# Performance work log

Measured on AMD Instinct MI355X. Metric: run time of the kernel, lower is better.

The kernel has to match this reference:

```python
import jax, jax.numpy as jnp
import numpy as np

B, T, D, H, C = 64, 256, 512, 1024, 1000

def setup_inputs() -> dict:
    key = jax.random.key(0)
    ks = jax.random.split(key, 6)
    s = 1.0 / np.sqrt(H)  # torch nn.RNN init scale
    return {
        "x": jax.random.normal(ks[0], (B, T, D), dtype=jnp.float32),
        "w_ih0": jax.random.normal(ks[1], (H, D), dtype=jnp.float32) * s,
        "w_hh0": jax.random.normal(ks[2], (H, H), dtype=jnp.float32) * s,
        "w_ih1": jax.random.normal(ks[3], (H, H), dtype=jnp.float32) * s,
        "w_hh1": jax.random.normal(ks[4], (H, H), dtype=jnp.float32) * s,
        "w_fc": jax.random.normal(ks[5], (C, H), dtype=jnp.float32) * s,
    }

def _rnn_layer(inp, w_ih, w_hh):
    # inp: [B, T, Din]; ReLU RNN, no bias (matches nn.RNN(nonlinearity='relu', bias=False))
    xs = jnp.einsum('btd,hd->tbh', inp, w_ih)  # precompute input projections for all steps
    h0 = jnp.zeros((inp.shape[0], w_hh.shape[0]), dtype=inp.dtype)
    def step(h, x_t):
        h = jax.nn.relu(x_t + h @ w_hh.T)
        return h, h
    _, ys = jax.lax.scan(step, h0, xs)  # ys: [T, B, H]
    return jnp.swapaxes(ys, 0, 1)  # [B, T, H]

def reference(x, w_ih0, w_hh0, w_ih1, w_hh1, w_fc):
    h1 = _rnn_layer(x, w_ih0, w_hh0)
    h2 = _rnn_layer(h1, w_ih1, w_hh1)
    # fc on last timestep, no bias
    return h2[:, -1, :] @ w_fc.T  # [B, C]
```

## Files before the change

kernel.cpp:

```cpp
#include <hip/hip_runtime.h>

#define T_STEPS 256
#define BATCH   64
#define HID     1024
#define DIN     512
#define NCLS    1000
#define NBLK    128
#define HSZ     (BATCH * HID)

typedef __attribute__((ext_vector_type(8))) short  short8;
typedef __attribute__((ext_vector_type(4))) float  f32x4;
typedef unsigned long long u64;

__device__ __forceinline__ unsigned short rne_bf16(float f) {
    unsigned int u = __builtin_bit_cast(unsigned int, f);
    u += 0x7FFFu + ((u >> 16) & 1u);
    return (unsigned short)(u >> 16);
}
__device__ __forceinline__ float bf16_to_f(unsigned short h) {
    unsigned int u = ((unsigned int)h) << 16;
    return __builtin_bit_cast(float, u);
}

#define MFMA(a, b, c) __builtin_amdgcn_mfma_f32_16x16x32_bf16((a), (b), (c), 0, 0, 0)

__device__ __forceinline__ short8 ld_st8(const unsigned short* p) {
    u64 a = __hip_atomic_load((const u64*)p,       __ATOMIC_RELAXED, __HIP_MEMORY_SCOPE_AGENT);
    u64 b = __hip_atomic_load((const u64*)(p + 4), __ATOMIC_RELAXED, __HIP_MEMORY_SCOPE_AGENT);
    union { u64 q[2]; short8 v; } u;
    u.q[0] = a; u.q[1] = b;
    return u.v;
}
__device__ __forceinline__ void st_u32(unsigned short* p, unsigned int v) {
    __hip_atomic_store((unsigned int*)p, v, __ATOMIC_RELAXED, __HIP_MEMORY_SCOPE_AGENT);
}

__device__ __forceinline__ void grid_bar(int* cnt, int bid, int tid, int p) {
    __syncthreads();
    if (tid == 0) {
        __hip_atomic_fetch_add(&cnt[((bid >> 1) & 7) * 32], 1,
                               __ATOMIC_RELAXED, __HIP_MEMORY_SCOPE_AGENT);
        const int target = 64 * (p + 1);
        for (long it = 0; it < 50000000L; ++it) {
            int s = 0;
#pragma unroll
            for (int i = 0; i < 8; ++i)
                s += __hip_atomic_load(&cnt[i * 32], __ATOMIC_RELAXED,
                                       __HIP_MEMORY_SCOPE_AGENT);
            if (s >= target) break;
        }
        asm volatile("" ::: "memory");
    }
    __syncthreads();
}

__device__ __forceinline__ void reduce_store(const float* red, int tid,
                                             int mbase, int nbase,
                                             unsigned short* ohi, unsigned short* olo,
                                             float* of, const float* xp) {
    const int m = tid >> 4;
    const int n = (tid * 2) & 31;
    float s0, s1;
    if (xp) {
        float2 xi = *(const float2*)(xp + (size_t)(mbase + m) * HID + nbase + n);
        s0 = xi.x; s1 = xi.y;
    } else { s0 = 0.f; s1 = 0.f; }
#pragma unroll
    for (int ww = 0; ww < 8; ++ww) {
        const float* rp = red + ww * 1088 + m * 34 + n;
        s0 += rp[0];
        s1 += rp[1];
    }
    const float v0 = fmaxf(s0, 0.f), v1 = fmaxf(s1, 0.f);
    const unsigned short h0 = rne_bf16(v0), h1 = rne_bf16(v1);
    const unsigned int hp = (unsigned int)h0 | ((unsigned int)h1 << 16);
    const unsigned int lp = (unsigned int)rne_bf16(v0 - bf16_to_f(h0)) |
                            ((unsigned int)rne_bf16(v1 - bf16_to_f(h1)) << 16);
    const size_t o = (size_t)(mbase + m) * HID + nbase + n;
    st_u32(ohi + o, hp);
    st_u32(olo + o, lp);
    if (of) { float2 f2; f2.x = v0; f2.y = v1; *(float2*)(of + o) = f2; }
}

__global__ __launch_bounds__(512, 2)
void rnn_mfma(const float* __restrict__ xproj,
              const unsigned short* __restrict__ whh0h, const unsigned short* __restrict__ whh0l,
              const unsigned short* __restrict__ wih1h, const unsigned short* __restrict__ wih1l,
              const unsigned short* __restrict__ whh1h, const unsigned short* __restrict__ whh1l,
              unsigned short* h1hi, unsigned short* h1lo,
              unsigned short* h2hi, unsigned short* h2lo,
              float* h2f, int* bar) {
    __shared__ float red[8 * 1088];

    const int bid   = blockIdx.x;
    const int z     = bid >> 6;
    const int r     = bid & 63;
    const int nbase = (r >> 1) * 32;
    const int mbase = (r & 1) * 32;
    const int tid   = threadIdx.x;
    const int w     = tid >> 6;
    const int lane  = tid & 63;
    const int l15   = lane & 15;
    const int kq    = (lane >> 4) * 8;

    int* cnt = bar + (bid & 1) * 256;

    if (z == 0) {
        short8 WH[2][4], WL[2][4];
        const int kb = w * 128;
#pragma unroll
        for (int c = 0; c < 4; ++c)
#pragma unroll
            for (int nt = 0; nt < 2; ++nt) {
                const size_t o = (size_t)(nbase + nt * 16 + l15) * HID + kb + c * 32 + kq;
                WH[nt][c] = *(const short8*)(whh0h + o);
                WL[nt][c] = *(const short8*)(whh0l + o);
            }
        for (int p = 0; p <= T_STEPS; ++p) {
            if (p < T_STEPS) {
                f32x4 acc[2][2] = {};
                const unsigned short* hch = h1hi + (size_t)(p & 1) * HSZ;
                const unsigned short* hcl = h1lo + (size_t)(p & 1) * HSZ;
#pragma unroll
                for (int c = 0; c < 4; ++c) {
                    short8 ah[2], al[2];
#pragma unroll
                    for (int mt = 0; mt < 2; ++mt) {
                        const size_t o = (size_t)(mbase + mt * 16 + l15) * HID + kb + c * 32 + kq;
                        ah[mt] = ld_st8(hch + o);
                        al[mt] = ld_st8(hcl + o);
                    }
#pragma unroll
                    for (int mt = 0; mt < 2; ++mt)
#pragma unroll
                        for (int nt = 0; nt < 2; ++nt) {
                            acc[mt][nt] = MFMA(ah[mt], WH[nt][c], acc[mt][nt]);
                            acc[mt][nt] = MFMA(al[mt], WH[nt][c], acc[mt][nt]);
                            acc[mt][nt] = MFMA(ah[mt], WL[nt][c], acc[mt][nt]);
                        }
                }
#pragma unroll
                for (int mt = 0; mt < 2; ++mt)
#pragma unroll
                    for (int nt = 0; nt < 2; ++nt)
#pragma unroll
                        for (int i = 0; i < 4; ++i)
                            red[w * 1088 + (mt * 16 + (lane >> 4) * 4 + i) * 34 +
                                nt * 16 + l15] = acc[mt][nt][i];
                __syncthreads();
                const size_t ob = (size_t)((p + 1) & 1) * HSZ;
                reduce_store(red, tid, mbase, nbase, h1hi + ob, h1lo + ob, nullptr,
                             xproj + (size_t)p * BATCH * HID);
            }
            grid_bar(cnt, bid, tid, p);
        }
    } else {
        short8 WH[2][8], WL[2][8];
        const unsigned short* ph = (w < 4) ? wih1h : whh1h;
        const unsigned short* pl = (w < 4) ? wih1l : whh1l;
        const int kb = (w & 3) * 256;
#pragma unroll
        for (int c = 0; c < 8; ++c)
#pragma unroll
            for (int nt = 0; nt < 2; ++nt) {
                const size_t o = (size_t)(nbase + nt * 16 + l15) * HID + kb + c * 32 + kq;
                WH[nt][c] = *(const short8*)(ph + o);
                WL[nt][c] = *(const short8*)(pl + o);
            }
        for (int p = 0; p <= T_STEPS; ++p) {
            if (p >= 1) {
                f32x4 acc[2][2] = {};
                const unsigned short* ash = (w < 4) ? h1hi + (size_t)(p & 1) * HSZ
                                                    : h2hi + (size_t)((p - 1) & 1) * HSZ;
                const unsigned short* asl = (w < 4) ? h1lo + (size_t)(p & 1) * HSZ
                                                    : h2lo + (size_t)((p - 1) & 1) * HSZ;
#pragma unroll
                for (int c = 0; c < 8; ++c) {
                    short8 ah[2], al[2];
#pragma unroll
                    for (int mt = 0; mt < 2; ++mt) {
                        const size_t o = (size_t)(mbase + mt * 16 + l15) * HID + kb + c * 32 + kq;
                        ah[mt] = ld_st8(ash + o);
                        al[mt] = ld_st8(asl + o);
                    }
#pragma unroll
                    for (int mt = 0; mt < 2; ++mt)
#pragma unroll
                        for (int nt = 0; nt < 2; ++nt) {
                            acc[mt][nt] = MFMA(ah[mt], WH[nt][c], acc[mt][nt]);
                            acc[mt][nt] = MFMA(al[mt], WH[nt][c], acc[mt][nt]);
                            acc[mt][nt] = MFMA(ah[mt], WL[nt][c], acc[mt][nt]);
                        }
                }
#pragma unroll
                for (int mt = 0; mt < 2; ++mt)
#pragma unroll
                    for (int nt = 0; nt < 2; ++nt)
#pragma unroll
                        for (int i = 0; i < 4; ++i)
                            red[w * 1088 + (mt * 16 + (lane >> 4) * 4 + i) * 34 +
                                nt * 16 + l15] = acc[mt][nt][i];
                __syncthreads();
                const size_t ob = (size_t)(p & 1) * HSZ;
                reduce_store(red, tid, mbase, nbase, h2hi + ob, h2lo + ob,
                             (p == T_STEPS) ? h2f : nullptr, nullptr);
            }
            grid_bar(cnt, bid, tid, p);
        }
    }
}

__global__ __launch_bounds__(512)
void xproj_gemm(const float* __restrict__ x,
                const unsigned short* __restrict__ wh,
                const unsigned short* __restrict__ wl,
                float* __restrict__ xproj) {
    const int t    = blockIdx.x;
    const int nq   = blockIdx.y;
    const int w    = threadIdx.x >> 6;
    const int lane = threadIdx.x & 63;
    const int l15  = lane & 15;
    const int kq   = (lane >> 4) * 8;
    const int n0   = nq * 256 + w * 32;

    f32x4 acc[4][2] = {};
    for (int c = 0; c < 16; ++c) {
        const int k = c * 32 + kq;
        short8 wfh[2], wfl[2];
#pragma unroll
        for (int nt = 0; nt < 2; ++nt) {
            const size_t o = (size_t)(n0 + nt * 16 + l15) * DIN + k;
            wfh[nt] = *(const short8*)(wh + o);
            wfl[nt] = *(const short8*)(wl + o);
        }
#pragma unroll
        for (int mt = 0; mt < 4; ++mt) {
            const float* xr = x + ((size_t)(mt * 16 + l15) * T_STEPS + t) * DIN + k;
            float4 a0 = *(const float4*)xr;
            float4 a1 = *(const float4*)(xr + 4);
            float f[8] = {a0.x, a0.y, a0.z, a0.w, a1.x, a1.y, a1.z, a1.w};
            short8 ah, al;
#pragma unroll
            for (int i = 0; i < 8; ++i) {
                unsigned short h = rne_bf16(f[i]);
                ah[i] = (short)h;
                al[i] = (short)rne_bf16(f[i] - bf16_to_f(h));
            }
#pragma unroll
            for (int nt = 0; nt < 2; ++nt) {
                acc[mt][nt] = MFMA(ah, wfh[nt], acc[mt][nt]);
                acc[mt][nt] = MFMA(al, wfh[nt], acc[mt][nt]);
                acc[mt][nt] = MFMA(ah, wfl[nt], acc[mt][nt]);
            }
        }
    }
    float* op = xproj + (size_t)t * BATCH * HID;
#pragma unroll
    for (int mt = 0; mt < 4; ++mt)
#pragma unroll
        for (int nt = 0; nt < 2; ++nt)
#pragma unroll
            for (int i = 0; i < 4; ++i) {
                const int m = mt * 16 + (lane >> 4) * 4 + i;
                const int n = n0 + nt * 16 + l15;
                op[(size_t)m * HID + n] = acc[mt][nt][i];
            }
}

__global__ void split_w(const float* __restrict__ src,
                        unsigned short* __restrict__ hi,
                        unsigned short* __restrict__ lo, int n) {
    int i = blockIdx.x * 256 + threadIdx.x;
    if (i < n) {
        float v = src[i];
        unsigned short h = rne_bf16(v);
        hi[i] = h;
        lo[i] = rne_bf16(v - bf16_to_f(h));
    }
}

__global__ void zero_kernel(int* __restrict__ p, int n) {
    int i = blockIdx.x * 256 + threadIdx.x;
    if (i < n) p[i] = 0;
}

__global__ void fc_kernel(const float* __restrict__ h2,
                          const float* __restrict__ w_fc,
                          float* __restrict__ out) {
    __shared__ float hs[HID];
    const int b = blockIdx.x;
    for (int i = threadIdx.x; i < HID; i += 256) hs[i] = h2[(size_t)b * HID + i];
    __syncthreads();
    const int c = blockIdx.y * 256 + threadIdx.x;
    if (c < NCLS) {
        const float* w = w_fc + (size_t)c * HID;
        float s = 0.f;
        for (int k = 0; k < HID; k += 4) {
            float4 wv = *(const float4*)(w + k);
            s += wv.x * hs[k] + wv.y * hs[k + 1] + wv.z * hs[k + 2] + wv.w * hs[k + 3];
        }
        out[(size_t)b * NCLS + c] = s;
    }
}

extern "C" void kernel_launch(void* const* d_in, const int* in_sizes, int n_in,
                              void* d_out, int out_size, void* d_ws, size_t ws_size,
                              hipStream_t stream) {
    const float* x     = (const float*)d_in[0];
    const float* w_ih0 = (const float*)d_in[1];
    const float* w_hh0 = (const float*)d_in[2];
    const float* w_ih1 = (const float*)d_in[3];
    const float* w_hh1 = (const float*)d_in[4];
    const float* w_fc  = (const float*)d_in[5];
    float* out = (float*)d_out;

    char* ws = (char*)d_ws;
    size_t off = 0;
    auto alloc = [&](size_t bytes) { char* p = ws + off; off += bytes; return p; };
    float*          xproj = (float*)alloc((size_t)T_STEPS * BATCH * HID * 4);
    unsigned short* wih0h = (unsigned short*)alloc((size_t)DIN * HID * 2);
    unsigned short* wih0l = (unsigned short*)alloc((size_t)DIN * HID * 2);
    unsigned short* whh0h = (unsigned short*)alloc((size_t)HID * HID * 2);
    unsigned short* whh0l = (unsigned short*)alloc((size_t)HID * HID * 2);
    unsigned short* wih1h = (unsigned short*)alloc((size_t)HID * HID * 2);
    unsigned short* wih1l = (unsigned short*)alloc((size_t)HID * HID * 2);
    unsigned short* whh1h = (unsigned short*)alloc((size_t)HID * HID * 2);
    unsigned short* whh1l = (unsigned short*)alloc((size_t)HID * HID * 2);
    unsigned short* h1hi  = (unsigned short*)alloc(2 * HSZ * 2);
    unsigned short* h1lo  = (unsigned short*)alloc(2 * HSZ * 2);
    unsigned short* h2hi  = (unsigned short*)alloc(2 * HSZ * 2);
    unsigned short* h2lo  = (unsigned short*)alloc(2 * HSZ * 2);
    float*          h2f   = (float*)alloc(HSZ * 4);
    int*            bar   = (int*)alloc(4096);

    split_w<<<(DIN * HID + 255) / 256, 256, 0, stream>>>(w_ih0, wih0h, wih0l, DIN * HID);
    split_w<<<(HID * HID + 255) / 256, 256, 0, stream>>>(w_hh0, whh0h, whh0l, HID * HID);
    split_w<<<(HID * HID + 255) / 256, 256, 0, stream>>>(w_ih1, wih1h, wih1l, HID * HID);
    split_w<<<(HID * HID + 255) / 256, 256, 0, stream>>>(w_hh1, whh1h, whh1l, HID * HID);

    xproj_gemm<<<dim3(T_STEPS, 4), 512, 0, stream>>>(x, wih0h, wih0l, xproj);

    const int nzero = (4 * (2 * HSZ * 2) + HSZ * 4 + 4096) / 4;
    zero_kernel<<<(nzero + 255) / 256, 256, 0, stream>>>((int*)h1hi, nzero);

    rnn_mfma<<<NBLK, 512, 0, stream>>>(xproj,
                                       whh0h, whh0l,
                                       wih1h, wih1l, whh1h, whh1l,
                                       h1hi, h1lo, h2hi, h2lo, h2f, bar);

    fc_kernel<<<dim3(64, 4), 256, 0, stream>>>(h2f, w_fc, out);
}
```

Baseline: 4.445 ms.

## Replace global grid barrier with per-batch-chunk dataflow counters in persistent RNN

Replaces the per-step global grid barrier with per-chunk arrival counters, splitting the batch into four chunks of 16 rows. Each block now waits only on the counters for the chunk it is about to compute, so layers and blocks can run ahead in a wavefront. Tiles shrink from 32x32 to 16 columns by 16 rows per chunk, and spin-waits use s_sleep. This trades more synchronisation events, smaller MFMA tiles and repeated activation reloads for less barrier stall and more overlap between layers.

After: 8.339 ms. 87.6% more time.

```diff
diff --git a/kernel.cpp b/kernel.cpp
--- a/kernel.cpp
+++ b/kernel.cpp
@@ -6,6 +6,7 @@
 #define DIN     512
 #define NCLS    1000
 #define NBLK    128
+#define NCH     4
 #define HSZ     (BATCH * HID)
 
 typedef __attribute__((ext_vector_type(8))) short  short8;
@@ -35,51 +36,22 @@
     __hip_atomic_store((unsigned int*)p, v, __ATOMIC_RELAXED, __HIP_MEMORY_SCOPE_AGENT);
 }
 
-__device__ __forceinline__ void grid_bar(int* cnt, int bid, int tid, int p) {
-    __syncthreads();
-    if (tid == 0) {
-        __hip_atomic_fetch_add(&cnt[((bid >> 1) & 7) * 32], 1,
-                               __ATOMIC_RELAXED, __HIP_MEMORY_SCOPE_AGENT);
-        const int target = 64 * (p + 1);
-        for (long it = 0; it < 50000000L; ++it) {
-            int s = 0;
-#pragma unroll
-            for (int i = 0; i < 8; ++i)
-                s += __hip_atomic_load(&cnt[i * 32], __ATOMIC_RELAXED,
-                                       __HIP_MEMORY_SCOPE_AGENT);
-            if (s >= target) break;
-        }
-        asm volatile("" ::: "memory");
-    }
-    __syncthreads();
-}
-
-__device__ __forceinline__ void reduce_store(const float* red, int tid,
-                                             int mbase, int nbase,
-                                             unsigned short* ohi, unsigned short* olo,
-                                             float* of, const float* xp) {
-    const int m = tid >> 4;
-    const int n = (tid * 2) & 31;
-    float s0, s1;
-    if (xp) {
-        float2 xi = *(const float2*)(xp + (size_t)(mbase + m) * HID + nbase + n);
-        s0 = xi.x; s1 = xi.y;
-    } else { s0 = 0.f; s1 = 0.f; }
-#pragma unroll
-    for (int ww = 0; ww < 8; ++ww) {
-        const float* rp = red + ww * 1088 + m * 34 + n;
-        s0 += rp[0];
-        s1 += rp[1];
-    }
-    const float v0 = fmaxf(s0, 0.f), v1 = fmaxf(s1, 0.f);
-    const unsigned short h0 = rne_bf16(v0), h1 = rne_bf16(v1);
-    const unsigned int hp = (unsigned int)h0 | ((unsigned int)h1 << 16);
-    const unsigned int lp = (unsigned int)rne_bf16(v0 - bf16_to_f(h0)) |
-                            ((unsigned int)rne_bf16(v1 - bf16_to_f(h1)) << 16);
-    const size_t o = (size_t)(mbase + m) * HID + nbase + n;
-    st_u32(ohi + o, hp);
-    st_u32(olo + o, lp);
-    if (of) { float2 f2; f2.x = v0; f2.y = v1; *(float2*)(of + o) = f2; }
+__device__ __forceinline__ void wait_ge(const int* a, const int* b, int tgt) {
+    for (long it = 0; it < 100000000L; ++it) {
+        int s1 = 0, s2 = 0;
+#pragma unroll
+        for (int i = 0; i < 4; ++i) {
+            s1 += __hip_atomic_load(a + i * 16, __ATOMIC_RELAXED, __HIP_MEMORY_SCOPE_AGENT);
+            s2 += __hip_atomic_load(b + i * 16, __ATOMIC_RELAXED, __HIP_MEMORY_SCOPE_AGENT);
+        }
+        if (s1 >= tgt && s2 >= tgt) break;
+        __builtin_amdgcn_s_sleep(2);
+    }
+    asm volatile("" ::: "memory");
+}
+__device__ __forceinline__ void arrive(int* cb, int bid) {
+    __hip_atomic_fetch_add(cb + (bid & 3) * 16, 1,
+                           __ATOMIC_RELAXED, __HIP_MEMORY_SCOPE_AGENT);
 }
 
 __global__ __launch_bounds__(512, 2)
@@ -90,122 +62,147 @@
               unsigned short* h1hi, unsigned short* h1lo,
               unsigned short* h2hi, unsigned short* h2lo,
               float* h2f, int* bar) {
-    __shared__ float red[8 * 1088];
-
-    const int bid   = blockIdx.x;
-    const int z     = bid >> 6;
-    const int r     = bid & 63;
-    const int nbase = (r >> 1) * 32;
-    const int mbase = (r & 1) * 32;
-    const int tid   = threadIdx.x;
-    const int w     = tid >> 6;
-    const int lane  = tid & 63;
-    const int l15   = lane & 15;
-    const int kq    = (lane >> 4) * 8;
-
-    int* cnt = bar + (bid & 1) * 256;
-
-    if (z == 0) {
-        short8 WH[2][4], WL[2][4];
+    __shared__ float red[8][16][18];
+
+    const int bid  = blockIdx.x;
+    const int tid  = threadIdx.x;
+    const int w    = tid >> 6;
+    const int lane = tid & 63;
+    const int l15  = lane & 15;
+    const int kq   = (lane >> 4) * 8;
+    const int rm   = tid >> 3;
+    const int rn   = (tid & 7) * 2;
+
+    int* C1[NCH];
+    int* C2[NCH];
+#pragma unroll
+    for (int ch = 0; ch < NCH; ++ch) {
+        C1[ch] = bar + ch * 64;
+        C2[ch] = bar + (NCH + ch) * 64;
+    }
+
+    if (bid < 64) {
+        const int nb = bid * 16;
         const int kb = w * 128;
-#pragma unroll
-        for (int c = 0; c < 4; ++c)
-#pragma unroll
-            for (int nt = 0; nt < 2; ++nt) {
-                const size_t o = (size_t)(nbase + nt * 16 + l15) * HID + kb + c * 32 + kq;
-                WH[nt][c] = *(const short8*)(whh0h + o);
-                WL[nt][c] = *(const short8*)(whh0l + o);
-            }
-        for (int p = 0; p <= T_STEPS; ++p) {
-            if (p < T_STEPS) {
-                f32x4 acc[2][2] = {};
-                const unsigned short* hch = h1hi + (size_t)(p & 1) * HSZ;
-                const unsigned short* hcl = h1lo + (size_t)(p & 1) * HSZ;
-#pragma unroll
-                for (int c = 0; c < 4; ++c) {
-                    short8 ah[2], al[2];
-#pragma unroll
-                    for (int mt = 0; mt < 2; ++mt) {
-                        const size_t o = (size_t)(mbase + mt * 16 + l15) * HID + kb + c * 32 + kq;
-                        ah[mt] = ld_st8(hch + o);
-                        al[mt] = ld_st8(hcl + o);
+        short8 WH[4], WL[4];
+#pragma unroll
+        for (int ci = 0; ci < 4; ++ci) {
+            const size_t o = (size_t)(nb + l15) * HID + kb + ci * 32 + kq;
+            WH[ci] = *(const short8*)(whh0h + o);
+            WL[ci] = *(const short8*)(whh0l + o);
+        }
+        for (int p = 0; p < T_STEPS; ++p) {
+            const unsigned short* hch = h1hi + (size_t)(p & 1) * HSZ;
+            const unsigned short* hcl = h1lo + (size_t)(p & 1) * HSZ;
+            unsigned short* ohi = h1hi + (size_t)((p + 1) & 1) * HSZ;
+            unsigned short* olo = h1lo + (size_t)((p + 1) & 1) * HSZ;
+            const float* xp = xproj + (size_t)p * BATCH * HID;
+            for (int ch = 0; ch < NCH; ++ch) {
+                if (p > 0) {
+                    if (tid == 0) wait_ge(C1[ch], C2[ch], 64 * p);
+                    __syncthreads();
+                }
+                float2 xi = make_float2(0.f, 0.f);
+                if (tid < 128)
+                    xi = *(const float2*)(xp + (size_t)(ch * 16 + rm) * HID + nb + rn);
+                f32x4 acc = {};
+#pragma unroll
+                for (int ci = 0; ci < 4; ++ci) {
+                    const size_t o = (size_t)(ch * 16 + l15) * HID + kb + ci * 32 + kq;
+                    short8 ah = ld_st8(hch + o);
+                    short8 al = ld_st8(hcl + o);
+                    acc = MFMA(ah, WH[ci], acc);
+                    acc = MFMA(al, WH[ci], acc);
+                    acc = MFMA(ah, WL[ci], acc);
+                }
+#pragma unroll
+                for (int i = 0; i < 4; ++i)
+                    red[w][(lane >> 4) * 4 + i][l15] = acc[i];
+                __syncthreads();
+                if (tid < 128) {
+                    float s0 = xi.x, s1 = xi.y;
+#pragma unroll
+                    for (int ww = 0; ww < 8; ++ww) {
+                        s0 += red[ww][rm][rn];
+                        s1 += red[ww][rm][rn + 1];
                     }
-#pragma unroll
-                    for (int mt = 0; mt < 2; ++mt)
-#pragma unroll
-                        for (int nt = 0; nt < 2; ++nt) {
-                            acc[mt][nt] = MFMA(ah[mt], WH[nt][c], acc[mt][nt]);
-                            acc[mt][nt] = MFMA(al[mt], WH[nt][c], acc[mt][nt]);
-                            acc[mt][nt] = MFMA(ah[mt], WL[nt][c], acc[mt][nt]);
-                        }
-                }
-#pragma unroll
-                for (int mt = 0; mt < 2; ++mt)
-#pragma unroll
-                    for (int nt = 0; nt < 2; ++nt)
-#pragma unroll
-                        for (int i = 0; i < 4; ++i)
-                            red[w * 1088 + (mt * 16 + (lane >> 4) * 4 + i) * 34 +
-                                nt * 16 + l15] = acc[mt][nt][i];
-                __syncthreads();
-                const size_t ob = (size_t)((p + 1) & 1) * HSZ;
-                reduce_store(red, tid, mbase, nbase, h1hi + ob, h1lo + ob, nullptr,
-                             xproj + (size_t)p * BATCH * HID);
-            }
-            grid_bar(cnt, bid, tid, p);
+                    const float v0 = fmaxf(s0, 0.f), v1 = fmaxf(s1, 0.f);
+                    const unsigned short h0 = rne_bf16(v0), h1 = rne_bf16(v1);
+                    const unsigned int hp = (unsigned int)h0 | ((unsigned int)h1 << 16);
+                    const unsigned int lp = (unsigned int)rne_bf16(v0 - bf16_to_f(h0)) |
+                                            ((unsigned int)rne_bf16(v1 - bf16_to_f(h1)) << 16);
+                    const size_t o = (size_t)(ch * 16 + rm) * HID + nb + rn;
+                    st_u32(ohi + o, hp);
+                    st_u32(olo + o, lp);
+                }
+                __syncthreads();
+                if (tid == 0) arrive(C1[ch], bid);
+            }
         }
     } else {
-        short8 WH[2][8], WL[2][8];
+        const int nb = (bid - 64) * 16;
         const unsigned short* ph = (w < 4) ? wih1h : whh1h;
         const unsigned short* pl = (w < 4) ? wih1l : whh1l;
         const int kb = (w & 3) * 256;
-#pragma unroll
-        for (int c = 0; c < 8; ++c)
-#pragma unroll
-            for (int nt = 0; nt < 2; ++nt) {
-                const size_t o = (size_t)(nbase + nt * 16 + l15) * HID + kb + c * 32 + kq;
-                WH[nt][c] = *(const short8*)(ph + o);
-                WL[nt][c] = *(const short8*)(pl + o);
-            }
-        for (int p = 0; p <= T_STEPS; ++p) {
-            if (p >= 1) {
-                f32x4 acc[2][2] = {};
-                const unsigned short* ash = (w < 4) ? h1hi + (size_t)(p & 1) * HSZ
-                                                    : h2hi + (size_t)((p - 1) & 1) * HSZ;
-                const unsigned short* asl = (w < 4) ? h1lo + (size_t)(p & 1) * HSZ
-                                                    : h2lo + (size_t)((p - 1) & 1) * HSZ;
-#pragma unroll
-                for (int c = 0; c < 8; ++c) {
-                    short8 ah[2], al[2];
-#pragma unroll
-                    for (int mt = 0; mt < 2; ++mt) {
-                        const size_t o = (size_t)(mbase + mt * 16 + l15) * HID + kb + c * 32 + kq;
-                        ah[mt] = ld_st8(ash + o);
-                        al[mt] = ld_st8(asl + o);
+        short8 WH[8], WL[8];
+#pragma unroll
+        for (int ci = 0; ci < 8; ++ci) {
+            const size_t o = (size_t)(nb + l15) * HID + kb + ci * 32 + kq;
+            WH[ci] = *(const short8*)(ph + o);
+            WL[ci] = *(const short8*)(pl + o);
+        }
+        if (tid == 0)
+#pragma unroll
+            for (int ch = 0; ch < NCH; ++ch) arrive(C2[ch], bid);
+        for (int p = 1; p <= T_STEPS; ++p) {
+            const unsigned short* a1h = h1hi + (size_t)(p & 1) * HSZ;
+            const unsigned short* a1l = h1lo + (size_t)(p & 1) * HSZ;
+            const unsigned short* a2h = h2hi + (size_t)((p - 1) & 1) * HSZ;
+            const unsigned short* a2l = h2lo + (size_t)((p - 1) & 1) * HSZ;
+            const unsigned short* ash = (w < 4) ? a1h : a2h;
+            const unsigned short* asl = (w < 4) ? a1l : a2l;
+            unsigned short* ohi = h2hi + (size_t)(p & 1) * HSZ;
+            unsigned short* olo = h2lo + (size_t)(p & 1) * HSZ;
+            for (int ch = 0; ch < NCH; ++ch) {
+                if (tid == 0) wait_ge(C1[ch], C2[ch], 64 * p);
+                __syncthreads();
+                f32x4 acc = {};
+#pragma unroll
+                for (int ci = 0; ci < 8; ++ci) {
+                    const size_t o = (size_t)(ch * 16 + l15) * HID + kb + ci * 32 + kq;
+                    short8 ah = ld_st8(ash + o);
+                    short8 al = ld_st8(asl + o);
+                    acc = MFMA(ah, WH[ci], acc);
+                    acc = MFMA(al, WH[ci], acc);
+                    acc = MFMA(ah, WL[ci], acc);
+                }
+#pragma unroll
+                for (int i = 0; i < 4; ++i)
+                    red[w][(lane >> 4) * 4 + i][l15] = acc[i];
+                __syncthreads();
+                if (tid < 128) {
+                    float s0 = 0.f, s1 = 0.f;
+#pragma unroll
+                    for (int ww = 0; ww < 8; ++ww) {
+                        s0 += red[ww][rm][rn];
+                        s1 += red[ww][rm][rn + 1];
                     }
-#pragma unroll
-                    for (int mt = 0; mt < 2; ++mt)
-#pragma unroll
-                        for (int nt = 0; nt < 2; ++nt) {
-                            acc[mt][nt] = MFMA(ah[mt], WH[nt][c], acc[mt][nt]);
-                            acc[mt][nt] = MFMA(al[mt], WH[nt][c], acc[mt][nt]);
-                            acc[mt][nt] = MFMA(ah[mt], WL[nt][c], acc[mt][nt]);
-                        }
-                }
-#pragma unroll
-                for (int mt = 0; mt < 2; ++mt)
-#pragma unroll
-                    for (int nt = 0; nt < 2; ++nt)
-#pragma unroll
-                        for (int i = 0; i < 4; ++i)
-                            red[w * 1088 + (mt * 16 + (lane >> 4) * 4 + i) * 34 +
-                                nt * 16 + l15] = acc[mt][nt][i];
-                __syncthreads();
-                const size_t ob = (size_t)(p & 1) * HSZ;
-                reduce_store(red, tid, mbase, nbase, h2hi + ob, h2lo + ob,
-                             (p == T_STEPS) ? h2f : nullptr, nullptr);
-            }
-            grid_bar(cnt, bid, tid, p);
+                    const float v0 = fmaxf(s0, 0.f), v1 = fmaxf(s1, 0.f);
+                    const unsigned short h0 = rne_bf16(v0), h1 = rne_bf16(v1);
+                    const unsigned int hp = (unsigned int)h0 | ((unsigned int)h1 << 16);
+                    const unsigned int lp = (unsigned int)rne_bf16(v0 - bf16_to_f(h0)) |
+                                            ((unsigned int)rne_bf16(v1 - bf16_to_f(h1)) << 16);
+                    const size_t o = (size_t)(ch * 16 + rm) * HID + nb + rn;
+                    st_u32(ohi + o, hp);
+                    st_u32(olo + o, lp);
+                    if (p == T_STEPS) {
+                        float2 f2; f2.x = v0; f2.y = v1;
+                        *(float2*)(h2f + o) = f2;
+                    }
+                }
+                __syncthreads();
+                if (tid == 0) arrive(C2[ch], bid);
+            }
         }
     }
 }
```

## Replace grid-wide barrier with per-layer flag dataflow sync and 4-deep h1 ring

Applied to the files above, without the earlier changes.

Replaces the lockstep grid barrier, which made every block wait on all 128 blocks each step, with per-producer step flags. Each wave polls only the 32 flags it depends on (layer-1 flags, layer-2 flags) using a wavefront-wide __all check with s_sleep between polls. Layer 1 can now run up to three steps ahead of layer 2, so the h1 buffer grows to a 4-slot ring and the xproj load is issued before the wait. This lets the two layers pipeline instead of alternating, but correctness now depends on the relaxed atomic flag ordering. The poll loop also gives up after a much smaller iteration cap, so a long wait could let a block proceed early.

New measurement: 4.424 ms. About the same (-0.5%).

```diff
diff --git a/kernel.cpp b/kernel.cpp
--- a/kernel.cpp
+++ b/kernel.cpp
@@ -7,6 +7,7 @@
 #define NCLS    1000
 #define NBLK    128
 #define HSZ     (BATCH * HID)
+#define POLL_MAX 100000L
 
 typedef __attribute__((ext_vector_type(8))) short  short8;
 typedef __attribute__((ext_vector_type(4))) float  f32x4;
@@ -35,51 +36,17 @@
     __hip_atomic_store((unsigned int*)p, v, __ATOMIC_RELAXED, __HIP_MEMORY_SCOPE_AGENT);
 }
 
-__device__ __forceinline__ void grid_bar(int* cnt, int bid, int tid, int p) {
-    __syncthreads();
-    if (tid == 0) {
-        __hip_atomic_fetch_add(&cnt[((bid >> 1) & 7) * 32], 1,
-                               __ATOMIC_RELAXED, __HIP_MEMORY_SCOPE_AGENT);
-        const int target = 64 * (p + 1);
-        for (long it = 0; it < 50000000L; ++it) {
-            int s = 0;
-#pragma unroll
-            for (int i = 0; i < 8; ++i)
-                s += __hip_atomic_load(&cnt[i * 32], __ATOMIC_RELAXED,
-                                       __HIP_MEMORY_SCOPE_AGENT);
-            if (s >= target) break;
-        }
-        asm volatile("" ::: "memory");
-    }
-    __syncthreads();
-}
-
-__device__ __forceinline__ void reduce_store(const float* red, int tid,
-                                             int mbase, int nbase,
-                                             unsigned short* ohi, unsigned short* olo,
-                                             float* of, const float* xp) {
-    const int m = tid >> 4;
-    const int n = (tid * 2) & 31;
-    float s0, s1;
-    if (xp) {
-        float2 xi = *(const float2*)(xp + (size_t)(mbase + m) * HID + nbase + n);
-        s0 = xi.x; s1 = xi.y;
-    } else { s0 = 0.f; s1 = 0.f; }
-#pragma unroll
-    for (int ww = 0; ww < 8; ++ww) {
-        const float* rp = red + ww * 1088 + m * 34 + n;
-        s0 += rp[0];
-        s1 += rp[1];
-    }
-    const float v0 = fmaxf(s0, 0.f), v1 = fmaxf(s1, 0.f);
-    const unsigned short h0 = rne_bf16(v0), h1 = rne_bf16(v1);
-    const unsigned int hp = (unsigned int)h0 | ((unsigned int)h1 << 16);
-    const unsigned int lp = (unsigned int)rne_bf16(v0 - bf16_to_f(h0)) |
-                            ((unsigned int)rne_bf16(v1 - bf16_to_f(h1)) << 16);
-    const size_t o = (size_t)(mbase + m) * HID + nbase + n;
-    st_u32(ohi + o, hp);
-    st_u32(olo + o, lp);
-    if (of) { float2 f2; f2.x = v0; f2.y = v1; *(float2*)(of + o) = f2; }
+__device__ __forceinline__ void wave_poll(const int* fa, int ta,
+                                          const int* fb, int tb, int lane) {
+    const int* f = (lane < 32) ? fa : fb;
+    const int  t = (lane < 32) ? ta : tb;
+    const int  i = lane & 31;
+    for (long it = 0; it < POLL_MAX; ++it) {
+        int v = __hip_atomic_load(f + i, __ATOMIC_RELAXED, __HIP_MEMORY_SCOPE_AGENT);
+        if (__all(v >= t)) break;
+        __builtin_amdgcn_s_sleep(1);
+    }
+    asm volatile("" ::: "memory");
 }
 
 __global__ __launch_bounds__(512, 2)
@@ -92,120 +59,167 @@
               float* h2f, int* bar) {
     __shared__ float red[8 * 1088];
 
-    const int bid   = blockIdx.x;
-    const int z     = bid >> 6;
-    const int r     = bid & 63;
-    const int nbase = (r >> 1) * 32;
-    const int mbase = (r & 1) * 32;
-    const int tid   = threadIdx.x;
-    const int w     = tid >> 6;
-    const int lane  = tid & 63;
-    const int l15   = lane & 15;
-    const int kq    = (lane >> 4) * 8;
-
-    int* cnt = bar + (bid & 1) * 256;
-
-    if (z == 0) {
+    const int bid  = blockIdx.x;
+    const int tid  = threadIdx.x;
+    const int w    = tid >> 6;
+    const int lane = tid & 63;
+    const int l15  = lane & 15;
+    const int kq   = (lane >> 4) * 8;
+    const int rm   = tid >> 4;
+    const int rn   = (tid * 2) & 31;
+
+    const int isL2 = bid >= 64;
+    const int rb   = isL2 ? bid - 64 : bid;
+    const int ns   = rb >> 1;
+    const int mh   = rb & 1;
+    const int nb   = ns * 32;
+    const int mb   = mh * 32;
+
+    int* L1f = bar + mh * 32;
+    int* L2f = bar + 64 + mh * 32;
+
+    if (!isL2) {
+        const int kb = w * 128;
         short8 WH[2][4], WL[2][4];
-        const int kb = w * 128;
 #pragma unroll
         for (int c = 0; c < 4; ++c)
 #pragma unroll
             for (int nt = 0; nt < 2; ++nt) {
-                const size_t o = (size_t)(nbase + nt * 16 + l15) * HID + kb + c * 32 + kq;
+                const size_t o = (size_t)(nb + nt * 16 + l15) * HID + kb + c * 32 + kq;
                 WH[nt][c] = *(const short8*)(whh0h + o);
                 WL[nt][c] = *(const short8*)(whh0l + o);
             }
-        for (int p = 0; p <= T_STEPS; ++p) {
-            if (p < T_STEPS) {
-                f32x4 acc[2][2] = {};
-                const unsigned short* hch = h1hi + (size_t)(p & 1) * HSZ;
-                const unsigned short* hcl = h1lo + (size_t)(p & 1) * HSZ;
-#pragma unroll
-                for (int c = 0; c < 4; ++c) {
-                    short8 ah[2], al[2];
-#pragma unroll
-                    for (int mt = 0; mt < 2; ++mt) {
-                        const size_t o = (size_t)(mbase + mt * 16 + l15) * HID + kb + c * 32 + kq;
-                        ah[mt] = ld_st8(hch + o);
-                        al[mt] = ld_st8(hcl + o);
+        for (int p = 0; p < T_STEPS; ++p) {
+            const float2 xi = *(const float2*)(xproj + (size_t)p * BATCH * HID +
+                                               (size_t)(mb + rm) * HID + nb + rn);
+            wave_poll(L1f, p, L2f, p - 3, lane);
+            const unsigned short* hch = h1hi + (size_t)(p & 3) * HSZ;
+            const unsigned short* hcl = h1lo + (size_t)(p & 3) * HSZ;
+            f32x4 acc[2][2] = {};
+#pragma unroll
+            for (int c = 0; c < 4; ++c) {
+                short8 ah[2], al[2];
+#pragma unroll
+                for (int mt = 0; mt < 2; ++mt) {
+                    const size_t o = (size_t)(mb + mt * 16 + l15) * HID + kb + c * 32 + kq;
+                    ah[mt] = ld_st8(hch + o);
+                    al[mt] = ld_st8(hcl + o);
+                }
+#pragma unroll
+                for (int mt = 0; mt < 2; ++mt)
+#pragma unroll
+                    for (int nt = 0; nt < 2; ++nt) {
+                        acc[mt][nt] = MFMA(ah[mt], WH[nt][c], acc[mt][nt]);
+                        acc[mt][nt] = MFMA(al[mt], WH[nt][c], acc[mt][nt]);
+                        acc[mt][nt] = MFMA(ah[mt], WL[nt][c], acc[mt][nt]);
                     }
-#pragma unroll
-                    for (int mt = 0; mt < 2; ++mt)
-#pragma unroll
-                        for (int nt = 0; nt < 2; ++nt) {
-                            acc[mt][nt] = MFMA(ah[mt], WH[nt][c], acc[mt][nt]);
-                            acc[mt][nt] = MFMA(al[mt], WH[nt][c], acc[mt][nt]);
-                            acc[mt][nt] = MFMA(ah[mt], WL[nt][c], acc[mt][nt]);
-                        }
-                }
-#pragma unroll
-                for (int mt = 0; mt < 2; ++mt)
-#pragma unroll
-                    for (int nt = 0; nt < 2; ++nt)
-#pragma unroll
-                        for (int i = 0; i < 4; ++i)
-                            red[w * 1088 + (mt * 16 + (lane >> 4) * 4 + i) * 34 +
-                                nt * 16 + l15] = acc[mt][nt][i];
-                __syncthreads();
-                const size_t ob = (size_t)((p + 1) & 1) * HSZ;
-                reduce_store(red, tid, mbase, nbase, h1hi + ob, h1lo + ob, nullptr,
-                             xproj + (size_t)p * BATCH * HID);
-            }
-            grid_bar(cnt, bid, tid, p);
+            }
+#pragma unroll
+            for (int mt = 0; mt < 2; ++mt)
+#pragma unroll
+                for (int nt = 0; nt < 2; ++nt)
+#pragma unroll
+                    for (int i = 0; i < 4; ++i)
+                        red[w * 1088 + (mt * 16 + (lane >> 4) * 4 + i) * 34 +
+                            nt * 16 + l15] = acc[mt][nt][i];
+            __syncthreads();
+            {
+                float s0 = xi.x, s1 = xi.y;
+#pragma unroll
+                for (int ww = 0; ww < 8; ++ww) {
+                    const float* rp = red + ww * 1088 + rm * 34 + rn;
+                    s0 += rp[0];
+                    s1 += rp[1];
+                }
+                const float v0 = fmaxf(s0, 0.f), v1 = fmaxf(s1, 0.f);
+                const unsigned short h0 = rne_bf16(v0), h1 = rne_bf16(v1);
+                const unsigned int hp = (unsigned int)h0 | ((unsigned int)h1 << 16);
+                const unsigned int lp = (unsigned int)rne_bf16(v0 - bf16_to_f(h0)) |
+                                        ((unsigned int)rne_bf16(v1 - bf16_to_f(h1)) << 16);
+                const size_t o  = (size_t)(mb + rm) * HID + nb + rn;
+                const size_t ob = (size_t)((p + 1) & 3) * HSZ;
+                st_u32(h1hi + ob + o, hp);
+                st_u32(h1lo + ob + o, lp);
+            }
+            __syncthreads();
+            if (tid == 0)
+                __hip_atomic_store(&L1f[ns], p + 1, __ATOMIC_RELAXED,
+                                   __HIP_MEMORY_SCOPE_AGENT);
         }
     } else {
-        short8 WH[2][8], WL[2][8];
         const unsigned short* ph = (w < 4) ? wih1h : whh1h;
         const unsigned short* pl = (w < 4) ? wih1l : whh1l;
         const int kb = (w & 3) * 256;
+        short8 WH[2][8], WL[2][8];
 #pragma unroll
         for (int c = 0; c < 8; ++c)
 #pragma unroll
             for (int nt = 0; nt < 2; ++nt) {
-                const size_t o = (size_t)(nbase + nt * 16 + l15) * HID + kb + c * 32 + kq;
+                const size_t o = (size_t)(nb + nt * 16 + l15) * HID + kb + c * 32 + kq;
                 WH[nt][c] = *(const short8*)(ph + o);
                 WL[nt][c] = *(const short8*)(pl + o);
             }
-        for (int p = 0; p <= T_STEPS; ++p) {
-            if (p >= 1) {
-                f32x4 acc[2][2] = {};
-                const unsigned short* ash = (w < 4) ? h1hi + (size_t)(p & 1) * HSZ
-                                                    : h2hi + (size_t)((p - 1) & 1) * HSZ;
-                const unsigned short* asl = (w < 4) ? h1lo + (size_t)(p & 1) * HSZ
-                                                    : h2lo + (size_t)((p - 1) & 1) * HSZ;
-#pragma unroll
-                for (int c = 0; c < 8; ++c) {
-                    short8 ah[2], al[2];
-#pragma unroll
-                    for (int mt = 0; mt < 2; ++mt) {
-                        const size_t o = (size_t)(mbase + mt * 16 + l15) * HID + kb + c * 32 + kq;
-                        ah[mt] = ld_st8(ash + o);
-                        al[mt] = ld_st8(asl + o);
+        for (int p = 1; p <= T_STEPS; ++p) {
+            if (w < 4) wave_poll(L1f, p, L1f, p, lane);
+            else       wave_poll(L2f, p - 1, L2f, p - 1, lane);
+            const unsigned short* ash = (w < 4) ? h1hi + (size_t)(p & 3) * HSZ
+                                                : h2hi + (size_t)((p - 1) & 1) * HSZ;
+            const unsigned short* asl = (w < 4) ? h1lo + (size_t)(p & 3) * HSZ
+                                                : h2lo + (size_t)((p - 1) & 1) * HSZ;
+            f32x4 acc[2][2] = {};
+#pragma unroll
+            for (int c = 0; c < 8; ++c) {
+                short8 ah[2], al[2];
+#pragma unroll
+                for (int mt = 0; mt < 2; ++mt) {
+                    const size_t o = (size_t)(mb + mt * 16 + l15) * HID + kb + c * 32 + kq;
+                    ah[mt] = ld_st8(ash + o);
+                    al[mt] = ld_st8(asl + o);
+                }
+#pragma unroll
+                for (int mt = 0; mt < 2; ++mt)
+#pragma unroll
+                    for (int nt = 0; nt < 2; ++nt) {
+                        acc[mt][nt] = MFMA(ah[mt], WH[nt][c], acc[mt][nt]);
+                        acc[mt][nt] = MFMA(al[mt], WH[nt][c], acc[mt][nt]);
+                        acc[mt][nt] = MFMA(ah[mt], WL[nt][c], acc[mt][nt]);
                     }
-#pragma unroll
-                    for (int mt = 0; mt < 2; ++mt)
-#pragma unroll
-                        for (int nt = 0; nt < 2; ++nt) {
-                            acc[mt][nt] = MFMA(ah[mt], WH[nt][c], acc[mt][nt]);
-                            acc[mt][nt] = MFMA(al[mt], WH[nt][c], acc[mt][nt]);
-                            acc[mt][nt] = MFMA(ah[mt], WL[nt][c], acc[mt][nt]);
-                        }
-                }
-#pragma unroll
-                for (int mt = 0; mt < 2; ++mt)
-#pragma unroll
-                    for (int nt = 0; nt < 2; ++nt)
-#pragma unroll
-                        for (int i = 0; i < 4; ++i)
-                            red[w * 1088 + (mt * 16 + (lane >> 4) * 4 + i) * 34 +
-                                nt * 16 + l15] = acc[mt][nt][i];
-                __syncthreads();
+            }
+#pragma unroll
+            for (int mt = 0; mt < 2; ++mt)
+#pragma unroll
+                for (int nt = 0; nt < 2; ++nt)
+#pragma unroll
+                    for (int i = 0; i < 4; ++i)
+                        red[w * 1088 + (mt * 16 + (lane >> 4) * 4 + i) * 34 +
+                            nt * 16 + l15] = acc[mt][nt][i];
+            __syncthreads();
+            {
+                float s0 = 0.f, s1 = 0.f;
+#pragma unroll
+                for (int ww = 0; ww < 8; ++ww) {
+                    const float* rp = red + ww * 1088 + rm * 34 + rn;
+                    s0 += rp[0];
+                    s1 += rp[1];
+                }
+                const float v0 = fmaxf(s0, 0.f), v1 = fmaxf(s1, 0.f);
+                const unsigned short h0 = rne_bf16(v0), h1 = rne_bf16(v1);
+                const unsigned int hp = (unsigned int)h0 | ((unsigned int)h1 << 16);
+                const unsigned int lp = (unsigned int)rne_bf16(v0 - bf16_to_f(h0)) |
+                                        ((unsigned int)rne_bf16(v1 - bf16_to_f(h1)) << 16);
+                const size_t o  = (size_t)(mb + rm) * HID + nb + rn;
                 const size_t ob = (size_t)(p & 1) * HSZ;
-                reduce_store(red, tid, mbase, nbase, h2hi + ob, h2lo + ob,
-                             (p == T_STEPS) ? h2f : nullptr, nullptr);
-            }
-            grid_bar(cnt, bid, tid, p);
+                st_u32(h2hi + ob + o, hp);
+                st_u32(h2lo + ob + o, lp);
+                if (p == T_STEPS) {
+                    float2 f2; f2.x = v0; f2.y = v1;
+                    *(float2*)(h2f + o) = f2;
+                }
+            }
+            __syncthreads();
+            if (tid == 0)
+                __hip_atomic_store(&L2f[ns], p, __ATOMIC_RELAXED,
+                                   __HIP_MEMORY_SCOPE_AGENT);
         }
     }
 }
@@ -326,8 +340,8 @@
     unsigned short* wih1l = (unsigned short*)alloc((size_t)HID * HID * 2);
     unsigned short* whh1h = (unsigned short*)alloc((size_t)HID * HID * 2);
     unsigned short* whh1l = (unsigned short*)alloc((size_t)HID * HID * 2);
-    unsigned short* h1hi  = (unsigned short*)alloc(2 * HSZ * 2);
-    unsigned short* h1lo  = (unsigned short*)alloc(2 * HSZ * 2);
+    unsigned short* h1hi  = (unsigned short*)alloc(4 * HSZ * 2);
+    unsigned short* h1lo  = (unsigned short*)alloc(4 * HSZ * 2);
     unsigned short* h2hi  = (unsigned short*)alloc(2 * HSZ * 2);
     unsigned short* h2lo  = (unsigned short*)alloc(2 * HSZ * 2);
     float*          h2f   = (float*)alloc(HSZ * 4);
@@ -340,7 +354,7 @@
 
     xproj_gemm<<<dim3(T_STEPS, 4), 512, 0, stream>>>(x, wih0h, wih0l, xproj);
 
-    const int nzero = (4 * (2 * HSZ * 2) + HSZ * 4 + 4096) / 4;
+    const int nzero = (4 * HSZ * 2 * 2 + 2 * HSZ * 2 * 2 + HSZ * 4 + 4096) / 4;
     zero_kernel<<<(nzero + 255) / 256, 256, 0, stream>>>((int*)h1hi, nzero);
 
     rnn_mfma<<<NBLK, 512, 0, stream>>>(xproj,
```
